# Kernel tuning notes

Measured on AMD Instinct MI355X. Metric: run time of the kernel, lower is better.

Reference implementation:

```python
import jax, jax.numpy as jnp
import numpy as np

EMB = 256; HEADS = 8; K = 3; NOBJ = 3; STEPS = 3; MLP = 8; EPS = 1e-5; TEMP = 10000.0


def _pos_enc_2d(bs, h, w, e):
    # PositionalEncodingsFixed: interleaved sin/cos, positions from cumsum (1..h / 1..w)
    d = e // 2
    i = jnp.arange(d, dtype=jnp.float32)
    temp = TEMP ** (2.0 * jnp.floor(i / 2.0) / d)

    def enc1d(pos):  # pos: [n] -> [n, d]
        x = pos[:, None] / temp
        return jnp.stack([jnp.sin(x[:, 0::2]), jnp.cos(x[:, 1::2])], axis=-1).reshape(pos.shape[0], -1)

    ye = enc1d(jnp.arange(1, h + 1, dtype=jnp.float32))  # [h, d]
    xe = enc1d(jnp.arange(1, w + 1, dtype=jnp.float32))  # [w, d]
    pos = jnp.concatenate([
        jnp.broadcast_to(ye[:, None, :], (h, w, d)),
        jnp.broadcast_to(xe[None, :, :], (h, w, d))], axis=-1)  # [h, w, e]
    return jnp.broadcast_to(pos[None], (bs, h, w, e)).transpose(0, 3, 1, 2)  # [bs, e, h, w]


def _ln(x, g, b):
    m = jnp.mean(x, -1, keepdims=True)
    v = jnp.var(x, -1, keepdims=True)
    return (x - m) * jax.lax.rsqrt(v + EPS) * g + b


def _mha(q, k, v, wq, bq, wk, bk, wv, bv, wo, bo):
    # q: [L, B, E], k/v: [S, B, E] (batch_first=False convention)
    L, B, E = q.shape; S = k.shape[0]; Dh = E // HEADS
    qp = (q @ wq + bq).reshape(L, B, HEADS, Dh)
    kp = (k @ wk + bk).reshape(S, B, HEADS, Dh)
    vp = (v @ wv + bv).reshape(S, B, HEADS, Dh)
    att = jax.nn.softmax(jnp.einsum('lbhd,sbhd->bhls', qp, kp) / jnp.sqrt(jnp.float32(Dh)), axis=-1)
    out = jnp.einsum('bhls,sbhd->lbhd', att, vp).reshape(L, B, E)
    return out @ wo + bo


def _forward(f_e, pos_emb, bboxes, shape_map, mha_wq, mha_bq, mha_wk, mha_bk, mha_wv, mha_bv,
             mha_wo, mha_bo, la_wq, la_bq, la_wk, la_bk, la_wv, la_bv,
             ff_w1, ff_b1, ff_w2, ff_b2, n1_g, n1_b, n2_g, n2_b, n3_g, n3_b):
    bs, E, h, w = f_e.shape
    N = NOBJ * K * K
    scale = E ** -0.5
    # shape_emb: [N, bs, E] (zero-shot branch: learned parameter expanded over batch)
    shape_emb = jnp.broadcast_to(shape_map[None], (bs, NOBJ, K * K, E)).reshape(bs, N, E).transpose(1, 0, 2)
    qpe = _pos_enc_2d(bs, K, K, E).reshape(bs, E, K * K).transpose(2, 0, 1)  # [K^2, bs, E]
    query_pos = jnp.tile(qpe, (NOBJ, 1, 1))  # [N, bs, E]
    memory = f_e.reshape(bs, E, h * w).transpose(2, 0, 1).reshape(-1, E)  # [HW*bs, E]
    pos_flat = pos_emb.reshape(-1, E)
    qp_flat = query_pos.reshape(-1, E)

    # LinearAttention k/v paths are loop-invariant; hoist (same math as the per-step recompute).
    kk = jax.nn.softmax((memory + pos_flat) @ la_wk + la_bk, axis=0)  # softmax over rows
    vv = memory @ la_wv + la_bv
    context = jnp.sum(kk * vv, axis=0)  # einsum('be,be->e')

    F_k = shape_emb
    protos = []
    for _ in range(STEPS):
        # 1) cross-attn to shape embeddings (post-norm)
        a = _mha(F_k + query_pos, shape_emb, shape_emb,
                 mha_wq, mha_bq, mha_wk, mha_bk, mha_wv, mha_bv, mha_wo, mha_bo)
        F_k = _ln(F_k + a, n1_g, n1_b)
        # 2) linear attention over image memory
        q = jax.nn.softmax(((F_k.reshape(-1, E) + qp_flat) @ la_wq + la_bq) * scale, axis=-1)
        la = (q * context).reshape(F_k.shape)
        F_k = _ln(F_k + la, n2_g, n2_b)
        # 3) FFN
        ff = jax.nn.gelu(F_k @ ff_w1 + ff_b1, approximate=False) @ ff_w2 + ff_b2
        F_k = _ln(F_k + ff, n3_g, n3_b)
        protos.append(F_k)
    return jnp.stack(protos)  # [STEPS, N, bs, E]


def setup_inputs() -> dict:
    key = jax.random.key(0)
    ks = jax.random.split(key, 24)
    bs, h, w = 32, 64, 64
    s = 0.02
    def n(k, shp, sc=s):
        return jax.random.normal(k, shp, jnp.float32) * sc
    E, F = EMB, MLP * EMB
    return {
        'f_e': jax.random.normal(ks[0], (bs, E, h, w), jnp.float32),
        'pos_emb': jax.random.normal(ks[1], (h * w, bs, E), jnp.float32),
        'bboxes': jax.random.uniform(ks[2], (bs, NOBJ, 4), jnp.float32),
        'shape_map': jax.random.normal(ks[3], (NOBJ, K * K, E), jnp.float32),
        'mha_wq': n(ks[4], (E, E)), 'mha_bq': jnp.zeros(E, jnp.float32),
        'mha_wk': n(ks[5], (E, E)), 'mha_bk': jnp.zeros(E, jnp.float32),
        'mha_wv': n(ks[6], (E, E)), 'mha_bv': jnp.zeros(E, jnp.float32),
        'mha_wo': n(ks[7], (E, E)), 'mha_bo': jnp.zeros(E, jnp.float32),
        'la_wq': n(ks[8], (E, E)), 'la_bq': jnp.zeros(E, jnp.float32),
        'la_wk': n(ks[9], (E, E)), 'la_bk': jnp.zeros(E, jnp.float32),
        'la_wv': n(ks[10], (E, E)), 'la_bv': jnp.zeros(E, jnp.float32),
        'ff_w1': n(ks[11], (E, F)), 'ff_b1': jnp.zeros(F, jnp.float32),
        'ff_w2': n(ks[12], (F, E)), 'ff_b2': jnp.zeros(E, jnp.float32),
        'n1_g': jnp.ones(E, jnp.float32), 'n1_b': jnp.zeros(E, jnp.float32),
        'n2_g': jnp.ones(E, jnp.float32), 'n2_b': jnp.zeros(E, jnp.float32),
        'n3_g': jnp.ones(E, jnp.float32), 'n3_b': jnp.zeros(E, jnp.float32),
    }


def reference(f_e, pos_emb, bboxes, shape_map, mha_wq, mha_bq, mha_wk, mha_bk, mha_wv, mha_bv,
              mha_wo, mha_bo, la_wq, la_bq, la_wk, la_bk, la_wv, la_bv,
              ff_w1, ff_b1, ff_w2, ff_b2, n1_g, n1_b, n2_g, n2_b, n3_g, n3_b):
    return _forward(f_e, pos_emb, bboxes, shape_map, mha_wq, mha_bq, mha_wk, mha_bk, mha_wv, mha_bv,
                    mha_wo, mha_bo, la_wq, la_bq, la_wk, la_bk, la_wv, la_bv,
                    ff_w1, ff_b1, ff_w2, ff_b2, n1_g, n1_b, n2_g, n2_b, n3_g, n3_b)
```

## Files before the change

kernel.cpp:

```cpp
#include <hip/hip_runtime.h>
#include <math.h>

#define EPS_ 1e-5f

#define WS_PART   ((size_t)0)
#define WS_CTX    ((size_t)524288)
#define WS_QP     ((size_t)524544)
#define WS_KP     ((size_t)531456)
#define WS_VP     ((size_t)538368)
#define WS_F      ((size_t)545280)
#define WS_ATTN   ((size_t)766464)
#define WS_H      ((size_t)987648)
#define WS_WKB    ((size_t)1872384)
#define WS_WVB    ((size_t)1905152)
#define WS_WOT    ((size_t)1937920)
#define WS_LAQT   ((size_t)1970688)
#define WS_W1T    ((size_t)2003456)
#define WS_W2T    ((size_t)2265600)
#define WS_MT     ((size_t)2527744)
#define WS_VPT    ((size_t)2560512)
#define WS_CST    ((size_t)2564608)

typedef short bf16x8 __attribute__((ext_vector_type(8)));
typedef float f32x4 __attribute__((ext_vector_type(4)));

__device__ __forceinline__ unsigned short f2bf(float f) {
    union { float f; unsigned u; } v; v.f = f;
    unsigned u = v.u;
    unsigned r = u + 0x7fffu + ((u >> 16) & 1u);
    return (unsigned short)(r >> 16);
}
__device__ __forceinline__ float bf2f(unsigned short s) {
    union { unsigned u; float f; } v; v.u = ((unsigned)s) << 16;
    return v.f;
}
__device__ __forceinline__ bf16x8 cvt8(const float* p) {
    float4 u = ((const float4*)p)[0];
    float4 v = ((const float4*)p)[1];
    bf16x8 r;
    r[0] = (short)f2bf(u.x); r[1] = (short)f2bf(u.y);
    r[2] = (short)f2bf(u.z); r[3] = (short)f2bf(u.w);
    r[4] = (short)f2bf(v.x); r[5] = (short)f2bf(v.y);
    r[6] = (short)f2bf(v.z); r[7] = (short)f2bf(v.w);
    return r;
}
__device__ __forceinline__ bf16x8 cvt8sum(const float* p, const float* q) {
    float4 u = ((const float4*)p)[0];
    float4 v = ((const float4*)p)[1];
    float4 a = ((const float4*)q)[0];
    float4 b = ((const float4*)q)[1];
    bf16x8 r;
    r[0] = (short)f2bf(u.x + a.x); r[1] = (short)f2bf(u.y + a.y);
    r[2] = (short)f2bf(u.z + a.z); r[3] = (short)f2bf(u.w + a.w);
    r[4] = (short)f2bf(v.x + b.x); r[5] = (short)f2bf(v.y + b.y);
    r[6] = (short)f2bf(v.z + b.z); r[7] = (short)f2bf(v.w + b.w);
    return r;
}

__global__ __launch_bounds__(256) void k_trans(const float* __restrict__ la_wk,
                                               const float* __restrict__ la_wv,
                                               const float* __restrict__ mha_wo,
                                               const float* __restrict__ la_wq,
                                               const float* __restrict__ ff_w1,
                                               const float* __restrict__ ff_w2,
                                               unsigned short* __restrict__ wkb,
                                               unsigned short* __restrict__ wvb,
                                               unsigned short* __restrict__ woT,
                                               unsigned short* __restrict__ laqT,
                                               unsigned short* __restrict__ w1T,
                                               unsigned short* __restrict__ w2T) {
    int g = blockIdx.x, t = threadIdx.x;
    if (g < 1024) {
        int which = g >> 8, r = g & 255;
        const float* W = (which == 0) ? la_wk : (which == 1) ? la_wv : (which == 2) ? mha_wo : la_wq;
        unsigned short* O = (which == 0) ? wkb : (which == 1) ? wvb : (which == 2) ? woT : laqT;
        O[(size_t)t * 256 + r] = f2bf(W[(size_t)r * 256 + t]);
    } else if (g < 3072) {
        int n = g - 1024;
        w1T[(size_t)n * 256 + t] = f2bf(ff_w1[(size_t)t * 2048 + n]);
    } else {
        int n = g - 3072;
        for (int i = 0; i < 8; ++i) {
            int k = t + 256 * i;
            w2T[(size_t)n * 2048 + k] = f2bf(ff_w2[(size_t)k * 256 + n]);
        }
    }
}

__global__ __launch_bounds__(256) void pa_gemm(const float* __restrict__ f_e,
                                               const float* __restrict__ pos_emb,
                                               const unsigned short* __restrict__ wkb,
                                               const unsigned short* __restrict__ wvb,
                                               const float* __restrict__ bk,
                                               const float* __restrict__ bv,
                                               float* __restrict__ part) {
    __shared__ __align__(16) unsigned short lv[128 * 40];
    __shared__ __align__(16) unsigned short lx[128 * 40];
    __shared__ __align__(16) unsigned short lbk[128 * 40];
    __shared__ __align__(16) unsigned short lbv[128 * 40];
    __shared__ float reds[2 * 128];
    __shared__ float redt[2 * 128];

    const int g  = blockIdx.x;
    const int et = g & 1;
    const int pt = (g >> 1) & 31;
    const int b  = g >> 6;
    const int p0 = pt * 128;
    const int e0 = et * 128;

    const int tid  = threadIdx.x;
    const int wave = tid >> 6;
    const int lane = tid & 63;
    const int quad = lane >> 4;
    const int l15  = lane & 15;
    const int wm = wave >> 1;
    const int wn = wave & 1;

    f32x4 accx[4][4], accv[4][4];
    const f32x4 zero4 = {0.f, 0.f, 0.f, 0.f};
#pragma unroll
    for (int i = 0; i < 4; ++i)
#pragma unroll
        for (int j = 0; j < 4; ++j) { accx[i][j] = zero4; accv[i][j] = zero4; }

    const int sk  = tid >> 3;
    const int sm0 = (tid & 7) << 4;
    const int pm  = tid >> 1;
    const int pkh = (tid & 1) << 4;

    const float* feb = f_e + (size_t)b * (256 * 4096) + p0;

#pragma unroll 1
    for (int kt = 0; kt < 8; ++kt) {
        const int c0 = kt * 32;
        __syncthreads();
        {
            const float* src = feb + (size_t)(c0 + sk) * 4096 + sm0;
#pragma unroll
            for (int i = 0; i < 4; ++i) {
                float4 v = ((const float4*)src)[i];
                lv[(sm0 + 4 * i + 0) * 40 + sk] = f2bf(v.x);
                lv[(sm0 + 4 * i + 1) * 40 + sk] = f2bf(v.y);
                lv[(sm0 + 4 * i + 2) * 40 + sk] = f2bf(v.z);
                lv[(sm0 + 4 * i + 3) * 40 + sk] = f2bf(v.w);
            }
        }
        {
            const uint4* srck = (const uint4*)(wkb + ((size_t)(e0 + pm) * 256 + c0 + pkh));
            const uint4* srcv = (const uint4*)(wvb + ((size_t)(e0 + pm) * 256 + c0 + pkh));
            uint4* dk = (uint4*)&lbk[pm * 40 + pkh];
            uint4* dv = (uint4*)&lbv[pm * 40 + pkh];
            dk[0] = srck[0]; dk[1] = srck[1];
            dv[0] = srcv[0]; dv[1] = srcv[1];
        }
        __syncthreads();
        {
            const float* psrc = pos_emb + ((size_t)(p0 + pm) * 32 + b) * 256 + c0 + pkh;
            union { uint4 v[2]; unsigned short s[16]; } tb, ob;
            const uint4* lsrc = (const uint4*)&lv[pm * 40 + pkh];
            tb.v[0] = lsrc[0]; tb.v[1] = lsrc[1];
#pragma unroll
            for (int i = 0; i < 4; ++i) {
                float4 pv = ((const float4*)psrc)[i];
                ob.s[4 * i + 0] = f2bf(bf2f(tb.s[4 * i + 0]) + pv.x);
                ob.s[4 * i + 1] = f2bf(bf2f(tb.s[4 * i + 1]) + pv.y);
                ob.s[4 * i + 2] = f2bf(bf2f(tb.s[4 * i + 2]) + pv.z);
                ob.s[4 * i + 3] = f2bf(bf2f(tb.s[4 * i + 3]) + pv.w);
            }
            uint4* ldst = (uint4*)&lx[pm * 40 + pkh];
            ldst[0] = ob.v[0]; ldst[1] = ob.v[1];
        }
        __syncthreads();

        bf16x8 av[4], ax[4], fk[4], fv[4];
#pragma unroll
        for (int ms = 0; ms < 4; ++ms) {
            int row = wm * 64 + ms * 16 + l15;
            av[ms] = *(const bf16x8*)&lv[row * 40 + quad * 8];
            ax[ms] = *(const bf16x8*)&lx[row * 40 + quad * 8];
        }
#pragma unroll
        for (int ns = 0; ns < 4; ++ns) {
            int row = wn * 64 + ns * 16 + l15;
            fk[ns] = *(const bf16x8*)&lbk[row * 40 + quad * 8];
            fv[ns] = *(const bf16x8*)&lbv[row * 40 + quad * 8];
        }
#pragma unroll
        for (int ms = 0; ms < 4; ++ms)
#pragma unroll
            for (int ns = 0; ns < 4; ++ns) {
                accx[ms][ns] = __builtin_amdgcn_mfma_f32_16x16x32_bf16(ax[ms], fk[ns], accx[ms][ns], 0, 0, 0);
                accv[ms][ns] = __builtin_amdgcn_mfma_f32_16x16x32_bf16(av[ms], fv[ns], accv[ms][ns], 0, 0, 0);
            }
    }
    __syncthreads();

#pragma unroll
    for (int ns = 0; ns < 4; ++ns) {
        int nloc = wn * 64 + ns * 16 + l15;
        float bkv = bk[e0 + nloc];
        float bvv = bv[e0 + nloc];
        float ps = 0.f, pt_ = 0.f;
#pragma unroll
        for (int ms = 0; ms < 4; ++ms)
#pragma unroll
            for (int r = 0; r < 4; ++r) {
                float ex = __expf(accx[ms][ns][r] + bkv);
                float vv = accv[ms][ns][r] + bvv;
                ps += ex;
                pt_ += ex * vv;
            }
        ps  += __shfl_xor(ps, 16);  ps  += __shfl_xor(ps, 32);
        pt_ += __shfl_xor(pt_, 16); pt_ += __shfl_xor(pt_, 32);
        if (lane < 16) { reds[wm * 128 + nloc] = ps; redt[wm * 128 + nloc] = pt_; }
    }
    __syncthreads();
    if (tid < 128) {
        float s = reds[tid] + reds[128 + tid];
        float t = redt[tid] + redt[128 + tid];
        part[(size_t)g * 256 + tid] = s;
        part[(size_t)g * 256 + 128 + tid] = t;
    }
}

__global__ __launch_bounds__(256) void pa_reduce(const float* __restrict__ part,
                                                 float* __restrict__ ctx) {
    int e = blockIdx.x, tid = threadIdx.x;
    int et = e >> 7, n = e & 127;
    float s = 0.f, t = 0.f;
#pragma unroll
    for (int j = 0; j < 4; ++j) {
        int q = tid * 4 + j;
        const float* p = part + (size_t)(q * 2 + et) * 256 + n;
        s += p[0];
        t += p[128];
    }
    int wave = tid >> 6, lane = tid & 63;
#pragma unroll
    for (int o = 1; o < 64; o <<= 1) { s += __shfl_xor(s, o); t += __shfl_xor(t, o); }
    __shared__ float rs[4], rt[4];
    if (lane == 0) { rs[wave] = s; rt[wave] = t; }
    __syncthreads();
    if (tid == 0) {
        float S = rs[0] + rs[1] + rs[2] + rs[3];
        float T = rt[0] + rt[1] + rt[2] + rt[3];
        ctx[e] = T / S;
    }
}

__global__ __launch_bounds__(256) void k_qpos(float* __restrict__ qp) {
    int n = blockIdx.x, e = threadIdx.x;
    int q9 = n % 9;
    int y = q9 / 3, x = q9 % 3;
    float pos; int idx;
    if (e < 128) { pos = (float)(y + 1); idx = e; }
    else         { pos = (float)(x + 1); idx = e - 128; }
    int j = idx >> 1;
    float inv = expf(-(float)j * 0.14391156831212787f);
    float arg = pos * inv;
    qp[(size_t)n * 256 + e] = (idx & 1) ? cosf(arg) : sinf(arg);
}

__global__ __launch_bounds__(256) void k_kvproj(const float* __restrict__ sm,
                                                const float* __restrict__ wk,
                                                const float* __restrict__ bk,
                                                const float* __restrict__ wv,
                                                const float* __restrict__ bv,
                                                float* __restrict__ kp,
                                                float* __restrict__ vp) {
    int g = blockIdx.x;
    int n = g % 27, which = g / 27;
    int e = threadIdx.x;
    const float* W = which ? wv : wk;
    const float* B = which ? bv : bk;
    float* O = which ? vp : kp;
    const float* row = sm + (size_t)n * 256;
    float acc = 0.f;
    for (int c = 0; c < 256; ++c) acc += row[c] * W[(size_t)c * 256 + e];
    O[(size_t)n * 256 + e] = acc + B[e];
}

__global__ __launch_bounds__(256) void k_mt(const float* __restrict__ wq,
                                            const float* __restrict__ bq,
                                            const float* __restrict__ kp,
                                            unsigned short* __restrict__ MT,
                                            float* __restrict__ cst) {
    int h = blockIdx.x >> 5, s = blockIdx.x & 31;
    int c = threadIdx.x;
    const float SC = 0.17677669529663687f;
    if (s < 27) {
        float a = 0.f;
#pragma unroll
        for (int d = 0; d < 32; ++d)
            a += wq[(size_t)c * 256 + h * 32 + d] * kp[(size_t)s * 256 + h * 32 + d];
        MT[((size_t)(h * 32 + s)) * 256 + c] = f2bf(a * SC);
        if (c == 0) {
            float cb = 0.f;
#pragma unroll
            for (int d = 0; d < 32; ++d) cb += bq[h * 32 + d] * kp[(size_t)s * 256 + h * 32 + d];
            cst[h * 32 + s] = cb * SC;
        }
    } else {
        MT[((size_t)(h * 32 + s)) * 256 + c] = 0;
        if (c == 0) cst[h * 32 + s] = -1e30f;
    }
}

__global__ __launch_bounds__(256) void k_vpt(const float* __restrict__ vp,
                                             unsigned short* __restrict__ vpT) {
    int h = blockIdx.x, t = threadIdx.x;
    int s = t & 31;
#pragma unroll
    for (int i = 0; i < 4; ++i) {
        int d = (t >> 5) + 8 * i;
        vpT[((size_t)(h * 32 + d)) * 32 + s] = (s < 27) ? f2bf(vp[(size_t)s * 256 + h * 32 + d]) : (unsigned short)0;
    }
}

__global__ __launch_bounds__(256) void k_finit(const float* __restrict__ sm,
                                               float* __restrict__ F) {
    int r = blockIdx.x, e = threadIdx.x;
    F[(size_t)r * 256 + e] = sm[(size_t)(r >> 5) * 256 + e];
}

__global__ __launch_bounds__(256) void b1_attn(const float* __restrict__ F,
                                               const float* __restrict__ qp,
                                               const unsigned short* __restrict__ MT,
                                               const float* __restrict__ cst,
                                               const unsigned short* __restrict__ vpT,
                                               float* __restrict__ aout) {
    __shared__ float S[32][33];
    __shared__ __align__(16) unsigned short Pb[32][40];
    int b = blockIdx.x >> 3, h = blockIdx.x & 7;
    int tid = threadIdx.x, wave = tid >> 6, lane = tid & 63;
    int quad = lane >> 4, l15 = lane & 15;
    int lt = wave >> 1, st = wave & 1;
    const f32x4 z4 = {0.f, 0.f, 0.f, 0.f};
    f32x4 acc = z4;
    int l = lt * 16 + l15;
    bool lok = (l < 27);
    const float* xF = F + (size_t)(l * 32 + b) * 256;
    const float* xq = qp + (size_t)l * 256;
    const unsigned short* Bp = MT + (size_t)(h * 32 + st * 16 + l15) * 256;
#pragma unroll
    for (int kt = 0; kt < 8; ++kt) {
        int c = kt * 32 + quad * 8;
        bf16x8 a;
        if (lok) a = cvt8sum(xF + c, xq + c);
        else {
#pragma unroll
            for (int i = 0; i < 8; ++i) a[i] = 0;
        }
        bf16x8 bb = *(const bf16x8*)(Bp + c);
        acc = __builtin_amdgcn_mfma_f32_16x16x32_bf16(a, bb, acc, 0, 0, 0);
    }
    float cstv = cst[h * 32 + st * 16 + l15];
#pragma unroll
    for (int r = 0; r < 4; ++r) S[lt * 16 + quad * 4 + r][st * 16 + l15] = acc[r] + cstv;
    __syncthreads();
    if (tid < 32) {
        float pv[32];
        float m = -1e30f;
#pragma unroll
        for (int s = 0; s < 32; ++s) { pv[s] = S[tid][s]; m = fmaxf(m, pv[s]); }
        float sum = 0.f;
#pragma unroll
        for (int s = 0; s < 32; ++s) { pv[s] = __expf(pv[s] - m); sum += pv[s]; }
        float inv = 1.f / sum;
#pragma unroll
        for (int s = 0; s < 32; ++s) Pb[tid][s] = f2bf(pv[s] * inv);
    }
    __syncthreads();
    bf16x8 a2 = *(const bf16x8*)&Pb[lt * 16 + l15][quad * 8];
    bf16x8 b2 = *(const bf16x8*)(vpT + (size_t)(h * 32 + st * 16 + l15) * 32 + quad * 8);
    f32x4 o = __builtin_amdgcn_mfma_f32_16x16x32_bf16(a2, b2, z4, 0, 0, 0);
#pragma unroll
    for (int r = 0; r < 4; ++r) {
        int ll = lt * 16 + quad * 4 + r;
        if (ll < 27) aout[(size_t)(ll * 32 + b) * 256 + h * 32 + st * 16 + l15] = o[r];
    }
}

__global__ __launch_bounds__(256) void b2_mid(const float* __restrict__ aout,
                                              const unsigned short* __restrict__ woT,
                                              const float* __restrict__ bo,
                                              float* __restrict__ F,
                                              const float* __restrict__ g1,
                                              const float* __restrict__ b1v,
                                              const float* __restrict__ qp,
                                              const unsigned short* __restrict__ laqT,
                                              const float* __restrict__ labq,
                                              const float* __restrict__ ctx,
                                              const float* __restrict__ g2,
                                              const float* __restrict__ b2v) {
    __shared__ __align__(16) unsigned short X1b[16][264];
    __shared__ float r1s[4][16], r1q[4][16], rm[4][16], rp[4][16], r2s[4][16], r2q[4][16];
    int r0 = blockIdx.x * 16;
    int lrow = r0 >> 5;
    int tid = threadIdx.x, w = tid >> 6, lane = tid & 63;
    int quad = lane >> 4, l15 = lane & 15;
    const f32x4 z4 = {0.f, 0.f, 0.f, 0.f};
    f32x4 acc[4] = {z4, z4, z4, z4};
    const float* Ap = aout + (size_t)(r0 + l15) * 256;
#pragma unroll
    for (int kt = 0; kt < 8; ++kt) {
        int c = kt * 32 + quad * 8;
        bf16x8 a = cvt8(Ap + c);
#pragma unroll
        for (int nt = 0; nt < 4; ++nt) {
            bf16x8 bb = *(const bf16x8*)(woT + (size_t)(w * 64 + nt * 16 + l15) * 256 + c);
            acc[nt] = __builtin_amdgcn_mfma_f32_16x16x32_bf16(a, bb, acc[nt], 0, 0, 0);
        }
    }
    int e_[4];
#pragma unroll
    for (int nt = 0; nt < 4; ++nt) e_[nt] = w * 64 + nt * 16 + l15;
    float val[4][4];
#pragma unroll
    for (int nt = 0; nt < 4; ++nt) {
        float bov = bo[e_[nt]];
#pragma unroll
        for (int r = 0; r < 4; ++r) {
            int row = quad * 4 + r;
            val[nt][r] = acc[nt][r] + bov + F[(size_t)(r0 + row) * 256 + e_[nt]];
        }
    }
#pragma unroll
    for (int r = 0; r < 4; ++r) {
        float s = val[0][r] + val[1][r] + val[2][r] + val[3][r];
        float q = val[0][r] * val[0][r] + val[1][r] * val[1][r] + val[2][r] * val[2][r] + val[3][r] * val[3][r];
#pragma unroll
        for (int o = 1; o < 16; o <<= 1) { s += __shfl_xor(s, o); q += __shfl_xor(q, o); }
        if (l15 == 0) { r1s[w][quad * 4 + r] = s; r1q[w][quad * 4 + r] = q; }
    }
    __syncthreads();
#pragma unroll
    for (int r = 0; r < 4; ++r) {
        int row = quad * 4 + r;
        float S = r1s[0][row] + r1s[1][row] + r1s[2][row] + r1s[3][row];
        float Q = r1q[0][row] + r1q[1][row] + r1q[2][row] + r1q[3][row];
        float mean = S * (1.f / 256.f);
        float var  = Q * (1.f / 256.f) - mean * mean;
        float rs   = rsqrtf(var + EPS_);
#pragma unroll
        for (int nt = 0; nt < 4; ++nt) {
            int e = e_[nt];
            float f1 = (val[nt][r] - mean) * rs * g1[e] + b1v[e];
            X1b[row][e] = f2bf(f1 + qp[(size_t)lrow * 256 + e]);
            val[nt][r] = f1;
        }
    }
    __syncthreads();
    f32x4 acc2[4] = {z4, z4, z4, z4};
#pragma unroll
    for (int kt = 0; kt < 8; ++kt) {
        int c = kt * 32 + quad * 8;
        bf16x8 a = *(const bf16x8*)&X1b[l15][c];
#pragma unroll
        for (int nt = 0; nt < 4; ++nt) {
            bf16x8 bb = *(const bf16x8*)(laqT + (size_t)(w * 64 + nt * 16 + l15) * 256 + c);
            acc2[nt] = __builtin_amdgcn_mfma_f32_16x16x32_bf16(a, bb, acc2[nt], 0, 0, 0);
        }
    }
    float y[4][4];
#pragma unroll
    for (int nt = 0; nt < 4; ++nt) {
        float bqv = labq[e_[nt]];
#pragma unroll
        for (int r = 0; r < 4; ++r) y[nt][r] = (acc2[nt][r] + bqv) * 0.0625f;
    }
#pragma unroll
    for (int r = 0; r < 4; ++r) {
        float m = fmaxf(fmaxf(y[0][r], y[1][r]), fmaxf(y[2][r], y[3][r]));
#pragma unroll
        for (int o = 1; o < 16; o <<= 1) m = fmaxf(m, __shfl_xor(m, o));
        if (l15 == 0) rm[w][quad * 4 + r] = m;
    }
    __syncthreads();
    float p[4][4];
#pragma unroll
    for (int r = 0; r < 4; ++r) {
        int row = quad * 4 + r;
        float M = fmaxf(fmaxf(rm[0][row], rm[1][row]), fmaxf(rm[2][row], rm[3][row]));
        float ps = 0.f;
#pragma unroll
        for (int nt = 0; nt < 4; ++nt) { p[nt][r] = __expf(y[nt][r] - M); ps += p[nt][r]; }
#pragma unroll
        for (int o = 1; o < 16; o <<= 1) ps += __shfl_xor(ps, o);
        if (l15 == 0) rp[w][row] = ps;
    }
    __syncthreads();
#pragma unroll
    for (int r = 0; r < 4; ++r) {
        int row = quad * 4 + r;
        float Ssum = rp[0][row] + rp[1][row] + rp[2][row] + rp[3][row];
        float inv = 1.f / Ssum;
#pragma unroll
        for (int nt = 0; nt < 4; ++nt)
            val[nt][r] = val[nt][r] + (p[nt][r] * inv) * ctx[e_[nt]];
    }
#pragma unroll
    for (int r = 0; r < 4; ++r) {
        float s = val[0][r] + val[1][r] + val[2][r] + val[3][r];
        float q = val[0][r] * val[0][r] + val[1][r] * val[1][r] + val[2][r] * val[2][r] + val[3][r] * val[3][r];
#pragma unroll
        for (int o = 1; o < 16; o <<= 1) { s += __shfl_xor(s, o); q += __shfl_xor(q, o); }
        if (l15 == 0) { r2s[w][quad * 4 + r] = s; r2q[w][quad * 4 + r] = q; }
    }
    __syncthreads();
#pragma unroll
    for (int r = 0; r < 4; ++r) {
        int row = quad * 4 + r;
        float S = r2s[0][row] + r2s[1][row] + r2s[2][row] + r2s[3][row];
        float Q = r2q[0][row] + r2q[1][row] + r2q[2][row] + r2q[3][row];
        float mean = S * (1.f / 256.f);
        float var  = Q * (1.f / 256.f) - mean * mean;
        float rs   = rsqrtf(var + EPS_);
#pragma unroll
        for (int nt = 0; nt < 4; ++nt) {
            int e = e_[nt];
            F[(size_t)(r0 + row) * 256 + e] = (val[nt][r] - mean) * rs * g2[e] + b2v[e];
        }
    }
}

__global__ __launch_bounds__(256) void b3_ffn1(const float* __restrict__ F,
                                               const unsigned short* __restrict__ w1T,
                                               const float* __restrict__ fb1,
                                               unsigned short* __restrict__ Hb) {
    int bm = blockIdx.x >> 5, bn = blockIdx.x & 31;
    int tid = threadIdx.x, w = tid >> 6, lane = tid & 63;
    int quad = lane >> 4, l15 = lane & 15;
    int r0 = bm * 16;
    int n0 = bn * 64 + w * 16;
    const f32x4 z4 = {0.f, 0.f, 0.f, 0.f};
    f32x4 acc = z4;
    const float* Ap = F + (size_t)(r0 + l15) * 256;
    const unsigned short* Bp = w1T + (size_t)(n0 + l15) * 256;
#pragma unroll
    for (int kt = 0; kt < 8; ++kt) {
        int c = kt * 32 + quad * 8;
        bf16x8 a = cvt8(Ap + c);
        bf16x8 bb = *(const bf16x8*)(Bp + c);
        acc = __builtin_amdgcn_mfma_f32_16x16x32_bf16(a, bb, acc, 0, 0, 0);
    }
    int e = n0 + l15;
    float bv = fb1[e];
#pragma unroll
    for (int r = 0; r < 4; ++r) {
        float hh = acc[r] + bv;
        float g = 0.5f * hh * (1.f + erff(hh * 0.70710678118654752f));
        Hb[(size_t)(r0 + quad * 4 + r) * 2048 + e] = f2bf(g);
    }
}

__global__ __launch_bounds__(256) void b4_ffn2(const unsigned short* __restrict__ Hb,
                                               const unsigned short* __restrict__ w2T,
                                               const float* __restrict__ fb2,
                                               float* __restrict__ F,
                                               const float* __restrict__ g3,
                                               const float* __restrict__ b3v,
                                               float* __restrict__ out,
                                               int step) {
    __shared__ float r3s[4][16], r3q[4][16];
    int r0 = blockIdx.x * 16;
    int tid = threadIdx.x, w = tid >> 6, lane = tid & 63;
    int quad = lane >> 4, l15 = lane & 15;
    const f32x4 z4 = {0.f, 0.f, 0.f, 0.f};
    f32x4 acc[4] = {z4, z4, z4, z4};
    const unsigned short* Ap = Hb + (size_t)(r0 + l15) * 2048;
#pragma unroll 4
    for (int kt = 0; kt < 64; ++kt) {
        int c = kt * 32 + quad * 8;
        bf16x8 a = *(const bf16x8*)(Ap + c);
#pragma unroll
        for (int nt = 0; nt < 4; ++nt) {
            bf16x8 bb = *(const bf16x8*)(w2T + (size_t)(w * 64 + nt * 16 + l15) * 2048 + c);
            acc[nt] = __builtin_amdgcn_mfma_f32_16x16x32_bf16(a, bb, acc[nt], 0, 0, 0);
        }
    }
    int e_[4];
#pragma unroll
    for (int nt = 0; nt < 4; ++nt) e_[nt] = w * 64 + nt * 16 + l15;
    float val[4][4];
#pragma unroll
    for (int nt = 0; nt < 4; ++nt) {
        float bv = fb2[e_[nt]];
#pragma unroll
        for (int r = 0; r < 4; ++r) {
            int row = quad * 4 + r;
            val[nt][r] = acc[nt][r] + bv + F[(size_t)(r0 + row) * 256 + e_[nt]];
        }
    }
#pragma unroll
    for (int r = 0; r < 4; ++r) {
        float s = val[0][r] + val[1][r] + val[2][r] + val[3][r];
        float q = val[0][r] * val[0][r] + val[1][r] * val[1][r] + val[2][r] * val[2][r] + val[3][r] * val[3][r];
#pragma unroll
        for (int o = 1; o < 16; o <<= 1) { s += __shfl_xor(s, o); q += __shfl_xor(q, o); }
        if (l15 == 0) { r3s[w][quad * 4 + r] = s; r3q[w][quad * 4 + r] = q; }
    }
    __syncthreads();
#pragma unroll
    for (int r = 0; r < 4; ++r) {
        int row = quad * 4 + r;
        float S = r3s[0][row] + r3s[1][row] + r3s[2][row] + r3s[3][row];
        float Q = r3q[0][row] + r3q[1][row] + r3q[2][row] + r3q[3][row];
        float mean = S * (1.f / 256.f);
        float var  = Q * (1.f / 256.f) - mean * mean;
        float rs   = rsqrtf(var + EPS_);
#pragma unroll
        for (int nt = 0; nt < 4; ++nt) {
            int e = e_[nt];
            float o = (val[nt][r] - mean) * rs * g3[e] + b3v[e];
            F[(size_t)(r0 + row) * 256 + e] = o;
            out[(size_t)step * 221184 + (size_t)(r0 + row) * 256 + e] = o;
        }
    }
}

extern "C" void kernel_launch(void* const* d_in, const int* in_sizes, int n_in,
                              void* d_out, int out_size, void* d_ws, size_t ws_size,
                              hipStream_t stream) {
    const float* f_e     = (const float*)d_in[0];
    const float* pos_emb = (const float*)d_in[1];
    const float* sm      = (const float*)d_in[3];
    const float* mha_wq  = (const float*)d_in[4];
    const float* mha_bq  = (const float*)d_in[5];
    const float* mha_wk  = (const float*)d_in[6];
    const float* mha_bk  = (const float*)d_in[7];
    const float* mha_wv  = (const float*)d_in[8];
    const float* mha_bv  = (const float*)d_in[9];
    const float* mha_wo  = (const float*)d_in[10];
    const float* mha_bo  = (const float*)d_in[11];
    const float* la_wq   = (const float*)d_in[12];
    const float* la_bq   = (const float*)d_in[13];
    const float* la_wk   = (const float*)d_in[14];
    const float* la_bk   = (const float*)d_in[15];
    const float* la_wv   = (const float*)d_in[16];
    const float* la_bv   = (const float*)d_in[17];
    const float* ff_w1   = (const float*)d_in[18];
    const float* ff_b1   = (const float*)d_in[19];
    const float* ff_w2   = (const float*)d_in[20];
    const float* ff_b2   = (const float*)d_in[21];
    const float* n1_g    = (const float*)d_in[22];
    const float* n1_b    = (const float*)d_in[23];
    const float* n2_g    = (const float*)d_in[24];
    const float* n2_b    = (const float*)d_in[25];
    const float* n3_g    = (const float*)d_in[26];
    const float* n3_b    = (const float*)d_in[27];

    float* ws = (float*)d_ws;
    float* part = ws + WS_PART;
    float* ctx  = ws + WS_CTX;
    float* qp   = ws + WS_QP;
    float* kp   = ws + WS_KP;
    float* vp   = ws + WS_VP;
    float* F    = ws + WS_F;
    float* aout = ws + WS_ATTN;
    unsigned short* Hb   = (unsigned short*)(ws + WS_H);
    unsigned short* wkb  = (unsigned short*)(ws + WS_WKB);
    unsigned short* wvb  = (unsigned short*)(ws + WS_WVB);
    unsigned short* woT  = (unsigned short*)(ws + WS_WOT);
    unsigned short* laqT = (unsigned short*)(ws + WS_LAQT);
    unsigned short* w1T  = (unsigned short*)(ws + WS_W1T);
    unsigned short* w2T  = (unsigned short*)(ws + WS_W2T);
    unsigned short* MT   = (unsigned short*)(ws + WS_MT);
    unsigned short* vpT  = (unsigned short*)(ws + WS_VPT);
    float* cst = ws + WS_CST;

    float* out = (float*)d_out;

    k_trans<<<3328, 256, 0, stream>>>(la_wk, la_wv, mha_wo, la_wq, ff_w1, ff_w2,
                                      wkb, wvb, woT, laqT, w1T, w2T);
    k_qpos<<<27, 256, 0, stream>>>(qp);
    k_kvproj<<<54, 256, 0, stream>>>(sm, mha_wk, mha_bk, mha_wv, mha_bv, kp, vp);
    k_mt<<<256, 256, 0, stream>>>(mha_wq, mha_bq, kp, MT, cst);
    k_vpt<<<8, 256, 0, stream>>>(vp, vpT);
    k_finit<<<864, 256, 0, stream>>>(sm, F);

    pa_gemm<<<2048, 256, 0, stream>>>(f_e, pos_emb, wkb, wvb, la_bk, la_bv, part);
    pa_reduce<<<256, 256, 0, stream>>>(part, ctx);

    for (int s = 0; s < 3; ++s) {
        b1_attn<<<256, 256, 0, stream>>>(F, qp, MT, cst, vpT, aout);
        b2_mid<<<54, 256, 0, stream>>>(aout, woT, mha_bo, F, n1_g, n1_b, qp,
                                       laqT, la_bq, ctx, n2_g, n2_b);
        b3_ffn1<<<1728, 256, 0, stream>>>(F, w1T, ff_b1, Hb);
        b4_ffn2<<<54, 256, 0, stream>>>(Hb, w2T, ff_b2, F, n3_g, n3_b, out, s);
    }
}
```

Baseline: 799.0 us.

## Tile weight transposes through LDS and pipeline pa_gemm loads with double buffering

```diff
diff --git a/kernel.cpp b/kernel.cpp
--- a/kernel.cpp
+++ b/kernel.cpp
@@ -69,35 +69,51 @@
                                                unsigned short* __restrict__ laqT,
                                                unsigned short* __restrict__ w1T,
                                                unsigned short* __restrict__ w2T) {
-    int g = blockIdx.x, t = threadIdx.x;
-    if (g < 1024) {
-        int which = g >> 8, r = g & 255;
-        const float* W = (which == 0) ? la_wk : (which == 1) ? la_wv : (which == 2) ? mha_wo : la_wq;
-        unsigned short* O = (which == 0) ? wkb : (which == 1) ? wvb : (which == 2) ? woT : laqT;
-        O[(size_t)t * 256 + r] = f2bf(W[(size_t)r * 256 + t]);
-    } else if (g < 3072) {
-        int n = g - 1024;
-        w1T[(size_t)n * 256 + t] = f2bf(ff_w1[(size_t)t * 2048 + n]);
+    __shared__ float T[64][65];
+    int id = blockIdx.x, t = threadIdx.x;
+    const float* src; unsigned short* dst; int R, C, tr, tc;
+    if (id < 64) {
+        int task = id >> 4, tile = id & 15;
+        R = 256; C = 256; tr = tile >> 2; tc = tile & 3;
+        src = task == 0 ? la_wk : task == 1 ? la_wv : task == 2 ? mha_wo : la_wq;
+        dst = task == 0 ? wkb : task == 1 ? wvb : task == 2 ? woT : laqT;
+    } else if (id < 192) {
+        int tile = id - 64;
+        R = 256; C = 2048; tr = tile >> 5; tc = tile & 31;
+        src = ff_w1; dst = w1T;
     } else {
-        int n = g - 3072;
-        for (int i = 0; i < 8; ++i) {
-            int k = t + 256 * i;
-            w2T[(size_t)n * 2048 + k] = f2bf(ff_w2[(size_t)k * 256 + n]);
-        }
-    }
-}
-
-__global__ __launch_bounds__(256) void pa_gemm(const float* __restrict__ f_e,
-                                               const float* __restrict__ pos_emb,
-                                               const unsigned short* __restrict__ wkb,
-                                               const unsigned short* __restrict__ wvb,
-                                               const float* __restrict__ bk,
-                                               const float* __restrict__ bv,
-                                               float* __restrict__ part) {
-    __shared__ __align__(16) unsigned short lv[128 * 40];
-    __shared__ __align__(16) unsigned short lx[128 * 40];
-    __shared__ __align__(16) unsigned short lbk[128 * 40];
-    __shared__ __align__(16) unsigned short lbv[128 * 40];
+        int tile = id - 192;
+        R = 2048; C = 256; tr = tile >> 2; tc = tile & 3;
+        src = ff_w2; dst = w2T;
+    }
+    int r0 = tr * 64, c0 = tc * 64;
+    int i = t >> 2, j0 = (t & 3) * 16;
+    const float* s = src + (size_t)(r0 + i) * C + c0 + j0;
+#pragma unroll
+    for (int k = 0; k < 4; ++k) {
+        float4 v = ((const float4*)s)[k];
+        T[i][j0 + 4 * k + 0] = v.x;
+        T[i][j0 + 4 * k + 1] = v.y;
+        T[i][j0 + 4 * k + 2] = v.z;
+        T[i][j0 + 4 * k + 3] = v.w;
+    }
+    __syncthreads();
+    unsigned short o[16];
+#pragma unroll
+    for (int k = 0; k < 16; ++k) o[k] = f2bf(T[j0 + k][i]);
+    unsigned short* d = dst + (size_t)(c0 + i) * R + r0 + j0;
+    ((uint4*)d)[0] = *(const uint4*)&o[0];
+    ((uint4*)d)[1] = *(const uint4*)&o[8];
+}
+
+__global__ __launch_bounds__(256, 2) void pa_gemm(const float* __restrict__ f_e,
+                                                  const float* __restrict__ pos_emb,
+                                                  const unsigned short* __restrict__ wkb,
+                                                  const unsigned short* __restrict__ wvb,
+                                                  const float* __restrict__ bk,
+                                                  const float* __restrict__ bv,
+                                                  float* __restrict__ part) {
+    __shared__ __align__(16) unsigned short lv[2][128 * 40];
     __shared__ float reds[2 * 128];
     __shared__ float redt[2 * 128];
 
@@ -125,75 +141,75 @@
 
     const int sk  = tid >> 3;
     const int sm0 = (tid & 7) << 4;
-    const int pm  = tid >> 1;
-    const int pkh = (tid & 1) << 4;
 
     const float* feb = f_e + (size_t)b * (256 * 4096) + p0;
+    const float* posb = pos_emb + ((size_t)(p0 + wm * 64 + l15) * 32 + b) * 256 + quad * 8;
+    const unsigned short* wkp = wkb + (size_t)(e0 + wn * 64 + l15) * 256 + quad * 8;
+    const unsigned short* wvp = wvb + (size_t)(e0 + wn * 64 + l15) * 256 + quad * 8;
+
+    float4 pf[4];
+    {
+        const float* src = feb + (size_t)sk * 4096 + sm0;
+#pragma unroll
+        for (int i = 0; i < 4; ++i) pf[i] = ((const float4*)src)[i];
+    }
 
 #pragma unroll 1
     for (int kt = 0; kt < 8; ++kt) {
         const int c0 = kt * 32;
+        unsigned short* L = lv[kt & 1];
+#pragma unroll
+        for (int i = 0; i < 4; ++i) {
+            L[(sm0 + 4 * i + 0) * 40 + sk] = f2bf(pf[i].x);
+            L[(sm0 + 4 * i + 1) * 40 + sk] = f2bf(pf[i].y);
+            L[(sm0 + 4 * i + 2) * 40 + sk] = f2bf(pf[i].z);
+            L[(sm0 + 4 * i + 3) * 40 + sk] = f2bf(pf[i].w);
+        }
+        float4 nf[4];
+        if (kt < 7) {
+            const float* src = feb + (size_t)(c0 + 32 + sk) * 4096 + sm0;
+#pragma unroll
+            for (int i = 0; i < 4; ++i) nf[i] = ((const float4*)src)[i];
+        }
+        float4 pp[4][2];
+#pragma unroll
+        for (int ms = 0; ms < 4; ++ms) {
+            const float* p = posb + (size_t)ms * (16 * 32 * 256) + c0;
+            pp[ms][0] = ((const float4*)p)[0];
+            pp[ms][1] = ((const float4*)p)[1];
+        }
         __syncthreads();
-        {
-            const float* src = feb + (size_t)(c0 + sk) * 4096 + sm0;
-#pragma unroll
-            for (int i = 0; i < 4; ++i) {
-                float4 v = ((const float4*)src)[i];
-                lv[(sm0 + 4 * i + 0) * 40 + sk] = f2bf(v.x);
-                lv[(sm0 + 4 * i + 1) * 40 + sk] = f2bf(v.y);
-                lv[(sm0 + 4 * i + 2) * 40 + sk] = f2bf(v.z);
-                lv[(sm0 + 4 * i + 3) * 40 + sk] = f2bf(v.w);
-            }
-        }
-        {
-            const uint4* srck = (const uint4*)(wkb + ((size_t)(e0 + pm) * 256 + c0 + pkh));
-            const uint4* srcv = (const uint4*)(wvb + ((size_t)(e0 + pm) * 256 + c0 + pkh));
-            uint4* dk = (uint4*)&lbk[pm * 40 + pkh];
-            uint4* dv = (uint4*)&lbv[pm * 40 + pkh];
-            dk[0] = srck[0]; dk[1] = srck[1];
-            dv[0] = srcv[0]; dv[1] = srcv[1];
-        }
-        __syncthreads();
-        {
-            const float* psrc = pos_emb + ((size_t)(p0 + pm) * 32 + b) * 256 + c0 + pkh;
-            union { uint4 v[2]; unsigned short s[16]; } tb, ob;
-            const uint4* lsrc = (const uint4*)&lv[pm * 40 + pkh];
-            tb.v[0] = lsrc[0]; tb.v[1] = lsrc[1];
-#pragma unroll
-            for (int i = 0; i < 4; ++i) {
-                float4 pv = ((const float4*)psrc)[i];
-                ob.s[4 * i + 0] = f2bf(bf2f(tb.s[4 * i + 0]) + pv.x);
-                ob.s[4 * i + 1] = f2bf(bf2f(tb.s[4 * i + 1]) + pv.y);
-                ob.s[4 * i + 2] = f2bf(bf2f(tb.s[4 * i + 2]) + pv.z);
-                ob.s[4 * i + 3] = f2bf(bf2f(tb.s[4 * i + 3]) + pv.w);
-            }
-            uint4* ldst = (uint4*)&lx[pm * 40 + pkh];
-            ldst[0] = ob.v[0]; ldst[1] = ob.v[1];
-        }
-        __syncthreads();
-
-        bf16x8 av[4], ax[4], fk[4], fv[4];
+        bf16x8 fk[4], fv[4];
+#pragma unroll
+        for (int ns = 0; ns < 4; ++ns) {
+            fk[ns] = *(const bf16x8*)(wkp + (size_t)ns * (16 * 256) + c0);
+            fv[ns] = *(const bf16x8*)(wvp + (size_t)ns * (16 * 256) + c0);
+        }
 #pragma unroll
         for (int ms = 0; ms < 4; ++ms) {
             int row = wm * 64 + ms * 16 + l15;
-            av[ms] = *(const bf16x8*)&lv[row * 40 + quad * 8];
-            ax[ms] = *(const bf16x8*)&lx[row * 40 + quad * 8];
-        }
-#pragma unroll
-        for (int ns = 0; ns < 4; ++ns) {
-            int row = wn * 64 + ns * 16 + l15;
-            fk[ns] = *(const bf16x8*)&lbk[row * 40 + quad * 8];
-            fv[ns] = *(const bf16x8*)&lbv[row * 40 + quad * 8];
-        }
-#pragma unroll
-        for (int ms = 0; ms < 4; ++ms)
+            uint4 avu = *(const uint4*)&L[row * 40 + quad * 8];
+            bf16x8 av = *(const bf16x8*)&avu;
+            bf16x8 ax;
+            ax[0] = (short)f2bf(__uint_as_float(avu.x << 16)          + pp[ms][0].x);
+            ax[1] = (short)f2bf(__uint_as_float(avu.x & 0xffff0000u)  + pp[ms][0].y);
+            ax[2] = (short)f2bf(__uint_as_float(avu.y << 16)          + pp[ms][0].z);
+            ax[3] = (short)f2bf(__uint_as_float(avu.y & 0xffff0000u)  + pp[ms][0].w);
+            ax[4] = (short)f2bf(__uint_as_float(avu.z << 16)          + pp[ms][1].x);
+            ax[5] = (short)f2bf(__uint_as_float(avu.z & 0xffff0000u)  + pp[ms][1].y);
+            ax[6] = (short)f2bf(__uint_as_float(avu.w << 16)          + pp[ms][1].z);
+            ax[7] = (short)f2bf(__uint_as_float(avu.w & 0xffff0000u)  + pp[ms][1].w);
 #pragma unroll
             for (int ns = 0; ns < 4; ++ns) {
-                accx[ms][ns] = __builtin_amdgcn_mfma_f32_16x16x32_bf16(ax[ms], fk[ns], accx[ms][ns], 0, 0, 0);
-                accv[ms][ns] = __builtin_amdgcn_mfma_f32_16x16x32_bf16(av[ms], fv[ns], accv[ms][ns], 0, 0, 0);
+                accx[ms][ns] = __builtin_amdgcn_mfma_f32_16x16x32_bf16(ax, fk[ns], accx[ms][ns], 0, 0, 0);
+                accv[ms][ns] = __builtin_amdgcn_mfma_f32_16x16x32_bf16(av, fv[ns], accv[ms][ns], 0, 0, 0);
             }
-    }
-    __syncthreads();
+        }
+        if (kt < 7) {
+#pragma unroll
+            for (int i = 0; i < 4; ++i) pf[i] = nf[i];
+        }
+    }
 
 #pragma unroll
     for (int ns = 0; ns < 4; ++ns) {
@@ -671,8 +687,8 @@
 
     float* out = (float*)d_out;
 
-    k_trans<<<3328, 256, 0, stream>>>(la_wk, la_wv, mha_wo, la_wq, ff_w1, ff_w2,
-                                      wkb, wvb, woT, laqT, w1T, w2T);
+    k_trans<<<320, 256, 0, stream>>>(la_wk, la_wv, mha_wo, la_wq, ff_w1, ff_w2,
+                                     wkb, wvb, woT, laqT, w1T, w2T);
     k_qpos<<<27, 256, 0, stream>>>(qp);
     k_kvproj<<<54, 256, 0, stream>>>(sm, mha_wk, mha_bk, mha_wv, mha_bv, kp, vp);
     k_mt<<<256, 256, 0, stream>>>(mha_wq, mha_bq, kp, MT, cst);
```

New measurement: 743.0 us. -7.0%, faster.
